# Optimization experiments

Measured on AMD Instinct MI355X. Metric: run time of the kernel, lower is better.

Reference implementation:

```python
import jax, jax.numpy as jnp
import numpy as np

VOCAB_SIZE = 256
CODEC_VOCAB = 1024  # 2 ** codec_bits
D = 1024
NHEAD = 16
FF = 4096
L = 6
ENROLLED = 225  # enrolled_codec_sec(3) * codec_rate(75)
B, TT, TA = 4, 128, 512


def sinusoidal_pe(T, d):
    pos = np.arange(T, dtype=np.float32)[:, None]
    div = np.exp(np.arange(0, d, 2, dtype=np.float32) * (-np.log(10000.0) / d))
    pe = np.zeros((T, d), dtype=np.float32)
    pe[:, 0::2] = np.sin(pos * div)
    pe[:, 1::2] = np.cos(pos * div)
    return jnp.asarray(pe)


def layernorm(x, w, b, eps=1e-5):
    mu = x.mean(-1, keepdims=True)
    var = ((x - mu) ** 2).mean(-1, keepdims=True)
    return (x - mu) * jax.lax.rsqrt(var + eps) * w + b


def mha(q_in, kv_in, in_w, in_b, out_w, out_b, mask=None):
    # q_in: [B,Tq,D], kv_in: [B,Tk,D]; mask True == blocked (torch attn_mask convention)
    d = q_in.shape[-1]
    h, hd = NHEAD, d // NHEAD
    wq, wk, wv = in_w[:d], in_w[d:2 * d], in_w[2 * d:]
    bq, bk, bv = in_b[:d], in_b[d:2 * d], in_b[2 * d:]
    Bq, Tq, _ = q_in.shape
    Tk = kv_in.shape[1]
    q = (q_in @ wq.T + bq).reshape(Bq, Tq, h, hd)
    k = (kv_in @ wk.T + bk).reshape(Bq, Tk, h, hd)
    v = (kv_in @ wv.T + bv).reshape(Bq, Tk, h, hd)
    scores = jnp.einsum('bqhd,bkhd->bhqk', q, k) / jnp.sqrt(jnp.float32(hd))
    if mask is not None:
        scores = jnp.where(mask, -jnp.inf, scores)
    attn = jax.nn.softmax(scores, axis=-1)
    o = jnp.einsum('bhqk,bkhd->bqhd', attn, v).reshape(Bq, Tq, d)
    return o @ out_w.T + out_b


def pack(te, ae, ee, tl, al):
    # Ragged concat [text[:tl]; audio[:al]; enrolled] padded to static max_len.
    Tt, Ta, Te = te.shape[0], ae.shape[0], ee.shape[0]
    pos = jnp.arange(Tt + Ta + Te)
    t = te[jnp.clip(pos, 0, Tt - 1)]
    a = ae[jnp.clip(pos - tl, 0, Ta - 1)]
    e = ee[jnp.clip(pos - tl - al, 0, Te - 1)]
    x = jnp.where((pos < tl)[:, None], t,
        jnp.where((pos < tl + al)[:, None], a,
        jnp.where((pos < tl + al + Te)[:, None], e, jnp.zeros_like(t))))
    return x


def setup_inputs():
    key = jax.random.key(0)
    ks = iter(jax.random.split(key, 64))

    def n(shape, s=0.02):
        return jax.random.normal(next(ks), shape, dtype=jnp.float32) * s

    text = jax.random.randint(next(ks), (B, TT), 0, VOCAB_SIZE)
    audio = jax.random.randint(next(ks), (B, TA), 0, CODEC_VOCAB)
    enrolled_audio = jax.random.randint(next(ks), (B, ENROLLED), 0, CODEC_VOCAB)
    # force sample 0 to full length so max_len is static (= TT+TA+ENROLLED)
    text_len_batch = jax.random.randint(next(ks), (B,), TT // 2, TT + 1).at[0].set(TT)
    audio_len_batch = jax.random.randint(next(ks), (B,), TA // 2, TA + 1).at[0].set(TA)
    return dict(
        text=text, audio=audio, enrolled_audio=enrolled_audio,
        text_len_batch=text_len_batch, audio_len_batch=audio_len_batch,
        text_emb=n((VOCAB_SIZE, D)), audio_emb=n((CODEC_VOCAB, D)),
        sa_in_w=n((L, 3 * D, D)), sa_in_b=jnp.zeros((L, 3 * D), jnp.float32),
        sa_out_w=n((L, D, D)), sa_out_b=jnp.zeros((L, D), jnp.float32),
        ca_in_w=n((L, 3 * D, D)), ca_in_b=jnp.zeros((L, 3 * D), jnp.float32),
        ca_out_w=n((L, D, D)), ca_out_b=jnp.zeros((L, D), jnp.float32),
        ff1_w=n((L, FF, D)), ff1_b=jnp.zeros((L, FF), jnp.float32),
        ff2_w=n((L, D, FF)), ff2_b=jnp.zeros((L, D), jnp.float32),
        ln1_w=jnp.ones((L, D), jnp.float32), ln1_b=jnp.zeros((L, D), jnp.float32),
        ln2_w=jnp.ones((L, D), jnp.float32), ln2_b=jnp.zeros((L, D), jnp.float32),
        ln3_w=jnp.ones((L, D), jnp.float32), ln3_b=jnp.zeros((L, D), jnp.float32),
        out_w=n((CODEC_VOCAB, D)), out_b=jnp.zeros((CODEC_VOCAB,), jnp.float32))


def reference(text, audio, enrolled_audio, text_len_batch, audio_len_batch,
              text_emb, audio_emb, sa_in_w, sa_in_b, sa_out_w, sa_out_b,
              ca_in_w, ca_in_b, ca_out_w, ca_out_b, ff1_w, ff1_b, ff2_w, ff2_b,
              ln1_w, ln1_b, ln2_w, ln2_b, ln3_w, ln3_b, out_w, out_b):
    # per-segment sinusoidal PE (positions reset at the start of each segment)
    te = text_emb[text] + sinusoidal_pe(text.shape[1], D)
    ae = audio_emb[audio] + sinusoidal_pe(audio.shape[1], D)
    ee = audio_emb[enrolled_audio] + sinusoidal_pe(enrolled_audio.shape[1], D)
    embed = jax.vmap(pack)(te, ae, ee, text_len_batch, audio_len_batch)  # [B, max_len, D]
    max_len = embed.shape[1]
    prefix = text.shape[1] + audio.shape[1]  # == max(tl+al) by construction
    mask = jnp.triu(jnp.ones((max_len, max_len), bool), 1).at[:, :prefix].set(False)
    mem = embed  # TransformerDecoder memory == embed
    x = embed
    for l in range(L):  # post-norm decoder layers (torch default norm_first=False)
        x = layernorm(x + mha(x, x, sa_in_w[l], sa_in_b[l], sa_out_w[l], sa_out_b[l], mask), ln1_w[l], ln1_b[l])
        x = layernorm(x + mha(x, mem, ca_in_w[l], ca_in_b[l], ca_out_w[l], ca_out_b[l]), ln2_w[l], ln2_b[l])
        h = jax.nn.relu(x @ ff1_w[l].T + ff1_b[l]) @ ff2_w[l].T + ff2_b[l]
        x = layernorm(x + h, ln3_w[l], ln3_b[l])
    return x @ out_w.T + out_b  # [B, max_len, CODEC_VOCAB]
```

## Files before the change

### kernel.cpp

```cpp
#include <hip/hip_runtime.h>
#include <hip/hip_bf16.h>

#define B_      4
#define TT_     128
#define TA_     512
#define TE_     225
#define T_      865
#define D_      1024
#define H_      16
#define FF_     4096
#define L_      6
#define PREFIX_ 640
#define M_TOK   (B_ * T_)
#define M_PAD   3584
#define NKV     (L_ * 2 * D_)

typedef __attribute__((ext_vector_type(8))) short          s16x8;
typedef __attribute__((ext_vector_type(4))) float          f32x4;
typedef __attribute__((ext_vector_type(8))) unsigned short u16x8;

typedef __attribute__((address_space(1))) const void gv_t;
typedef __attribute__((address_space(3))) void       lv_t;

__device__ __forceinline__ float bf2f(unsigned short u) {
  union { unsigned int i; float f; } c; c.i = ((unsigned int)u) << 16; return c.f;
}
__device__ __forceinline__ unsigned short f2bf(float f) {
  union { __hip_bfloat16 h; unsigned short u; } c; c.h = __float2bfloat16(f); return c.u;
}
template <int N> __device__ __forceinline__ void vmwait() {
  asm volatile("s_waitcnt vmcnt(%0)" :: "n"(N) : "memory");
}

__global__ __launch_bounds__(256) void embed_kernel(
    const int* __restrict__ text, const int* __restrict__ audio,
    const int* __restrict__ enrolled, const int* __restrict__ tl_b,
    const int* __restrict__ al_b, const float* __restrict__ text_emb,
    const float* __restrict__ audio_emb,
    float* __restrict__ xf, unsigned short* __restrict__ xb,
    unsigned short* __restrict__ memb, unsigned short* __restrict__ attnb) {
  int row = blockIdx.x;
  int d0 = threadIdx.x * 4;
  size_t off = (size_t)row * D_ + d0;
  if (row >= M_TOK) {
    *(unsigned long long*)&xb[off]    = 0ull;
    *(unsigned long long*)&memb[off]  = 0ull;
    *(unsigned long long*)&attnb[off] = 0ull;
    return;
  }
  int b = row / T_, pos = row - b * T_;
  int tl = tl_b[b], al = al_b[b];
  const float* emb = nullptr;
  int p = 0;
  if (pos < tl) {
    emb = text_emb + (size_t)text[b * TT_ + pos] * D_;
    p = pos;
  } else if (pos < tl + al) {
    emb = audio_emb + (size_t)audio[b * TA_ + (pos - tl)] * D_;
    p = pos - tl;
  } else if (pos < tl + al + TE_) {
    emb = audio_emb + (size_t)enrolled[b * TE_ + (pos - tl - al)] * D_;
    p = pos - tl - al;
  }
  float4 v;
  float* pv = (float*)&v;
  if (emb) {
    const float c = -9.2103403719761836f / (float)D_;
    #pragma unroll
    for (int e = 0; e < 4; ++e) {
      int d = d0 + e;
      int i = d >> 1;
      float freq = expf(c * (float)(2 * i));
      float arg = (float)p * freq;
      float pe = (d & 1) ? cosf(arg) : sinf(arg);
      pv[e] = emb[d] + pe;
    }
  } else {
    v = make_float4(0.f, 0.f, 0.f, 0.f);
  }
  *(float4*)&xf[off] = v;
  unsigned long long pk = (unsigned long long)f2bf(pv[0])
      | ((unsigned long long)f2bf(pv[1]) << 16)
      | ((unsigned long long)f2bf(pv[2]) << 32)
      | ((unsigned long long)f2bf(pv[3]) << 48);
  *(unsigned long long*)&xb[off]   = pk;
  *(unsigned long long*)&memb[off] = pk;
}

__global__ __launch_bounds__(256) void cvt_kernel(
    const float* __restrict__ in, unsigned short* __restrict__ out, int n8) {
  int i = blockIdx.x * 256 + threadIdx.x;
  if (i >= n8) return;
  const float4* pp = (const float4*)in + (size_t)i * 2;
  float4 a = pp[0], bq = pp[1];
  u16x8 o;
  o[0] = f2bf(a.x);  o[1] = f2bf(a.y);  o[2] = f2bf(a.z);  o[3] = f2bf(a.w);
  o[4] = f2bf(bq.x); o[5] = f2bf(bq.y); o[6] = f2bf(bq.z); o[7] = f2bf(bq.w);
  *(u16x8*)(out + (size_t)i * 8) = o;
}

__global__ __launch_bounds__(256) void cvt_layer_kernel(
    const float* __restrict__ s0, const float* __restrict__ s1,
    const float* __restrict__ s2, const float* __restrict__ s3,
    const float* __restrict__ s4, const float* __restrict__ s5,
    unsigned short* __restrict__ dst) {
  size_t e = ((size_t)blockIdx.x * 256 + threadIdx.x) * 8;
  if (e >= 16777216u) return;
  const float* src; size_t off;
  if      (e <  3145728u) { src = s0; off = e; }
  else if (e <  4194304u) { src = s1; off = e -  3145728u; }
  else if (e <  7340032u) { src = s2; off = e -  4194304u; }
  else if (e <  8388608u) { src = s3; off = e -  7340032u; }
  else if (e < 12582912u) { src = s4; off = e -  8388608u; }
  else                    { src = s5; off = e - 12582912u; }
  const float4* pp = (const float4*)(src + off);
  float4 a = pp[0], bq = pp[1];
  u16x8 o;
  o[0] = f2bf(a.x);  o[1] = f2bf(a.y);  o[2] = f2bf(a.z);  o[3] = f2bf(a.w);
  o[4] = f2bf(bq.x); o[5] = f2bf(bq.y); o[6] = f2bf(bq.z); o[7] = f2bf(bq.w);
  *(u16x8*)(dst + e) = o;
}

__global__ __launch_bounds__(256) void cvt_ckv_w(
    const float* __restrict__ ca_in_w, unsigned short* __restrict__ wckv) {
  int rr = blockIdx.x;
  int l = rr / (2 * D_), w = rr % (2 * D_);
  const float* src = ca_in_w + (size_t)l * 3 * D_ * D_ + (size_t)(D_ + w) * D_;
  unsigned short* dst = wckv + (size_t)rr * D_;
  int c = threadIdx.x * 4;
  float4 v4 = *(const float4*)(src + c);
  unsigned long long pk = (unsigned long long)f2bf(v4.x)
      | ((unsigned long long)f2bf(v4.y) << 16)
      | ((unsigned long long)f2bf(v4.z) << 32)
      | ((unsigned long long)f2bf(v4.w) << 48);
  *(unsigned long long*)&dst[c] = pk;
}

__global__ __launch_bounds__(256) void cvt_ckv_b(
    const float* __restrict__ ca_in_b, float* __restrict__ cbias) {
  int rr = blockIdx.x * 256 + threadIdx.x;
  if (rr >= NKV) return;
  int l = rr / (2 * D_), w = rr % (2 * D_);
  cbias[rr] = ca_in_b[(size_t)l * 3 * D_ + D_ + w];
}

template <int BM, int BN, int BK, int ACT, int OBF>
__global__ __launch_bounds__(256) void gemm_p2(
    const unsigned short* __restrict__ A, int lda,
    const unsigned short* __restrict__ W, int ldw,
    const float* __restrict__ bias,
    float* __restrict__ Cf, unsigned short* __restrict__ Cb, int ldc,
    int Mw, int K) {
  constexpr int WROWS = BM / 2, WCOLS = BN / 2;
  constexpr int WM = WROWS / 16, WN = WCOLS / 16;
  constexpr int LPR = BK / 8;
  constexpr int RPI = 64 / LPR;
  constexpr int ACH = (BM / 4) / RPI;
  constexpr int BCH = (BN / 4) / RPI;
  constexpr int ABUF = BM * BK, BBUF = BN * BK;
  constexpr int KSUB = BK / 32;
  constexpr int LW = ACH + BCH;
  __shared__ unsigned short lds[3 * (ABUF + BBUF)];

  int tid = threadIdx.x, lane = tid & 63, wid = tid >> 6;
  int gx = gridDim.x;
  int nwg = gx * gridDim.y;
  int orig = blockIdx.y * gx + blockIdx.x;
  int q = nwg >> 3, r = nwg & 7;
  int xcd = orig & 7, loc = orig >> 3;
  int wg = (xcd < r ? xcd * (q + 1) : r * (q + 1) + (xcd - r) * q) + loc;
  int m0 = (wg / gx) * BM, n0 = (wg % gx) * BN;

  int wr = wid >> 1, wc = wid & 1;
  int lrow = lane / LPR, lgrp = lane % LPR;
  int skey = (BK == 32) ? ((lrow >> 1) & 3) : (lrow & 7);
  int lk = (lgrp ^ skey) * 8;

  const unsigned short* gAp[ACH]; unsigned aoff[ACH];
  const unsigned short* gBp[BCH]; unsigned boff[BCH];
  #pragma unroll
  for (int c = 0; c < ACH; ++c) {
    int row0 = wid * (BM / 4) + c * RPI;
    gAp[c] = A + (size_t)(m0 + row0 + lrow) * lda + lk;
    aoff[c] = row0 * BK;
  }
  #pragma unroll
  for (int c = 0; c < BCH; ++c) {
    int row0 = wid * (BN / 4) + c * RPI;
    gBp[c] = W + (size_t)(n0 + row0 + lrow) * ldw + lk;
    boff[c] = row0 * BK;
  }

  f32x4 acc[WM][WN];
  #pragma unroll
  for (int i = 0; i < WM; ++i)
    #pragma unroll
    for (int j = 0; j < WN; ++j) acc[i][j] = (f32x4)0.f;

  int frow = lane & 15, g4 = lane >> 4;

  auto STAGE = [&](int bi, int t) {
    int k0 = t * BK;
    #pragma unroll
    for (int c = 0; c < ACH; ++c)
      __builtin_amdgcn_global_load_lds((gv_t*)(gAp[c] + k0),
          (lv_t*)&lds[bi * ABUF + aoff[c]], 16, 0, 0);
    #pragma unroll
    for (int c = 0; c < BCH; ++c)
      __builtin_amdgcn_global_load_lds((gv_t*)(gBp[c] + k0),
          (lv_t*)&lds[3 * ABUF + bi * BBUF + boff[c]], 16, 0, 0);
  };

  STAGE(0, 0);
  STAGE(1, 1);
  int nt = K / BK;
  int cur = 0;
  for (int t = 0; t < nt; ++t) {
    if (t + 1 < nt) vmwait<LW>(); else vmwait<0>();
    __builtin_amdgcn_s_barrier();
    if (t + 2 < nt) {
      int stb = cur + 2; if (stb >= 3) stb -= 3;
      STAGE(stb, t + 2);
    }
    const unsigned short* Ab = &lds[cur * ABUF];
    const unsigned short* Bb = &lds[3 * ABUF + cur * BBUF];
    #pragma unroll
    for (int kk = 0; kk < KSUB; ++kk) {
      int rk = (BK == 32) ? ((g4 ^ ((frow >> 1) & 3)) * 8)
                          : (((kk * 4 + g4) ^ (frow & 7)) * 8);
      s16x8 af[WM], bfr[WN];
      #pragma unroll
      for (int i = 0; i < WM; ++i)
        af[i] = *(const s16x8*)&Ab[(wr * WROWS + i * 16 + frow) * BK + rk];
      #pragma unroll
      for (int j = 0; j < WN; ++j)
        bfr[j] = *(const s16x8*)&Bb[(wc * WCOLS + j * 16 + frow) * BK + rk];
      __builtin_amdgcn_s_setprio(1);
      #pragma unroll
      for (int i = 0; i < WM; ++i)
        #pragma unroll
        for (int j = 0; j < WN; ++j)
          acc[i][j] = __builtin_amdgcn_mfma_f32_16x16x32_bf16(af[i], bfr[j], acc[i][j], 0, 0, 0);
      __builtin_amdgcn_s_setprio(0);
    }
    cur = (cur == 2) ? 0 : cur + 1;
  }

  float bv[WN];
  #pragma unroll
  for (int j = 0; j < WN; ++j) bv[j] = bias[n0 + wc * WCOLS + j * 16 + (lane & 15)];
  int rbase = m0 + wr * WROWS + (lane >> 4) * 4;
  int cbase = n0 + wc * WCOLS + (lane & 15);
  #pragma unroll
  for (int i = 0; i < WM; ++i)
    #pragma unroll
    for (int rr = 0; rr < 4; ++rr) {
      int m = rbase + i * 16 + rr;
      if (m < Mw) {
        #pragma unroll
        for (int j = 0; j < WN; ++j) {
          float v = acc[i][j][rr] + bv[j];
          if (ACT) v = fmaxf(v, 0.f);
          if (OBF) Cb[(size_t)m * ldc + cbase + j * 16] = f2bf(v);
          else     Cf[(size_t)m * ldc + cbase + j * 16] = v;
        }
      }
    }
}

template <bool MASKED>
__global__ __launch_bounds__(256) void attn_mfma(
    const unsigned short* __restrict__ qp, int qld,
    const unsigned short* __restrict__ kp,
    const unsigned short* __restrict__ vp, int kvld,
    unsigned short* __restrict__ out) {
  __shared__ unsigned short KsL[64 * 64];
  __shared__ unsigned short VtL[64 * 72];
  __shared__ unsigned short PsL[4][16 * 64];
  int tid = threadIdx.x;
  int lane = tid & 63, wid = tid >> 6;
  int b = blockIdx.y >> 4, h = blockIdx.y & 15;
  int q0 = blockIdx.x * 64;
  int r16 = lane & 15, g4 = lane >> 4;

  int qrow = q0 + wid * 16 + r16;
  if (qrow >= T_) qrow = T_ - 1;
  const unsigned short* qbase =
      qp + (size_t)(b * T_ + qrow) * qld + h * 64 + g4 * 8;
  s16x8 qf0 = *(const s16x8*)qbase;
  s16x8 qf1 = *(const s16x8*)(qbase + 32);

  float m_[4], l_[4];
  f32x4 o_[4];
  #pragma unroll
  for (int rg = 0; rg < 4; ++rg) { m_[rg] = -INFINITY; l_[rg] = 0.f; }
  #pragma unroll
  for (int dj = 0; dj < 4; ++dj) o_[dj] = (f32x4)0.f;

  const int nt = MASKED ? max(10, (int)blockIdx.x + 1) : 14;

  for (int t = 0; t < nt; ++t) {
    int k0 = t * 64;
    __syncthreads();

    #pragma unroll
    for (int c = 0; c < 2; ++c) {
      int row = wid * 16 + c * 8 + (lane >> 3);
      int kr = k0 + row; if (kr >= T_) kr = T_ - 1;
      int grp = (lane & 7) ^ (row & 7);
      const unsigned short* src =
          kp + (size_t)(b * T_ + kr) * kvld + h * 64 + grp * 8;
      __builtin_amdgcn_global_load_lds((gv_t*)src,
          (lv_t*)&KsL[(wid * 16 + c * 8) * 64], 16, 0, 0);
    }
    {
      int vkr = k0 + lane; if (vkr >= T_) vkr = T_ - 1;
      const unsigned short* vsrc =
          vp + (size_t)(b * T_ + vkr) * kvld + h * 64 + wid * 16;
      u16x8 v0 = *(const u16x8*)vsrc;
      u16x8 v1 = *(const u16x8*)(vsrc + 8);
      #pragma unroll
      for (int jj = 0; jj < 8; ++jj) {
        VtL[(wid * 16 + jj) * 72 + lane]     = v0[jj];
        VtL[(wid * 16 + 8 + jj) * 72 + lane] = v1[jj];
      }
    }
    __syncthreads();

    f32x4 sj[4];
    #pragma unroll
    for (int j = 0; j < 4; ++j) sj[j] = (f32x4)0.f;
    __builtin_amdgcn_s_setprio(1);
    #pragma unroll
    for (int j = 0; j < 4; ++j) {
      int krow = j * 16 + r16;
      s16x8 kf0 = *(const s16x8*)&KsL[krow * 64 + ((g4 ^ (krow & 7)) * 8)];
      s16x8 kf1 = *(const s16x8*)&KsL[krow * 64 + (((4 + g4) ^ (krow & 7)) * 8)];
      sj[j] = __builtin_amdgcn_mfma_f32_16x16x32_bf16(qf0, kf0, sj[j], 0, 0, 0);
      sj[j] = __builtin_amdgcn_mfma_f32_16x16x32_bf16(qf1, kf1, sj[j], 0, 0, 0);
    }
    __builtin_amdgcn_s_setprio(0);

    float alpha_[4];
    #pragma unroll
    for (int rg = 0; rg < 4; ++rg) {
      int qa = q0 + wid * 16 + g4 * 4 + rg;
      float pm = -INFINITY;
      #pragma unroll
      for (int j = 0; j < 4; ++j) {
        int kg = k0 + j * 16 + r16;
        float sv = sj[j][rg] * 0.125f;
        bool bad = (kg >= T_) || (MASKED && kg > qa && kg >= PREFIX_);
        sv = bad ? -INFINITY : sv;
        sj[j][rg] = sv;
        pm = fmaxf(pm, sv);
      }
      pm = fmaxf(pm, __shfl_xor(pm, 1));
      pm = fmaxf(pm, __shfl_xor(pm, 2));
      pm = fmaxf(pm, __shfl_xor(pm, 4));
      pm = fmaxf(pm, __shfl_xor(pm, 8));
      float mn = fmaxf(m_[rg], pm);
      float al = __expf(m_[rg] - mn);
      m_[rg] = mn;
      alpha_[rg] = al;
      int prow = g4 * 4 + rg;
      float ps = 0.f;
      #pragma unroll
      for (int j = 0; j < 4; ++j) {
        float pv = __expf(sj[j][rg] - mn);
        ps += pv;
        PsL[wid][prow * 64 + (((j * 2 + (r16 >> 3)) ^ (prow & 7)) * 8) + (r16 & 7)]
            = f2bf(pv);
      }
      ps += __shfl_xor(ps, 1);
      ps += __shfl_xor(ps, 2);
      ps += __shfl_xor(ps, 4);
      ps += __shfl_xor(ps, 8);
      l_[rg] = l_[rg] * al + ps;
    }
    #pragma unroll
    for (int dj = 0; dj < 4; ++dj)
      #pragma unroll
      for (int rg = 0; rg < 4; ++rg) o_[dj][rg] *= alpha_[rg];

    __builtin_amdgcn_s_setprio(1);
    #pragma unroll
    for (int kk = 0; kk < 2; ++kk) {
      s16x8 pf = *(const s16x8*)
          &PsL[wid][r16 * 64 + (((kk * 4 + g4) ^ (r16 & 7)) * 8)];
      #pragma unroll
      for (int dj = 0; dj < 4; ++dj) {
        s16x8 vf = *(const s16x8*)
            &VtL[(dj * 16 + r16) * 72 + kk * 32 + g4 * 8];
        o_[dj] = __builtin_amdgcn_mfma_f32_16x16x32_bf16(pf, vf, o_[dj], 0, 0, 0);
      }
    }
    __builtin_amdgcn_s_setprio(0);
  }

  #pragma unroll
  for (int rg = 0; rg < 4; ++rg) {
    int qa = q0 + wid * 16 + g4 * 4 + rg;
    if (qa < T_) {
      float inv = 1.f / l_[rg];
      unsigned short* ob = out + (size_t)(b * T_ + qa) * D_ + h * 64;
      #pragma unroll
      for (int dj = 0; dj < 4; ++dj)
        ob[dj * 16 + r16] = f2bf(o_[dj][rg] * inv);
    }
  }
}

__global__ __launch_bounds__(256) void ln_res_kernel(
    float* __restrict__ x, const float* __restrict__ r,
    const float* __restrict__ w, const float* __restrict__ b,
    unsigned short* __restrict__ xb) {
  __shared__ float red[4];
  int row = blockIdx.x, tid = threadIdx.x;
  size_t off = (size_t)row * D_ + tid * 4;
  float4 xv = *(float4*)&x[off];
  float4 rv = *(const float4*)&r[off];
  float v0 = xv.x + rv.x, v1 = xv.y + rv.y, v2 = xv.z + rv.z, v3 = xv.w + rv.w;

  float s = v0 + v1 + v2 + v3;
  #pragma unroll
  for (int o = 1; o < 64; o <<= 1) s += __shfl_xor(s, o);
  if ((tid & 63) == 0) red[tid >> 6] = s;
  __syncthreads();
  float mu = (red[0] + red[1] + red[2] + red[3]) * (1.f / 1024.f);
  __syncthreads();

  float d0 = v0 - mu, d1 = v1 - mu, d2 = v2 - mu, d3 = v3 - mu;
  float ss = d0 * d0 + d1 * d1 + d2 * d2 + d3 * d3;
  #pragma unroll
  for (int o = 1; o < 64; o <<= 1) ss += __shfl_xor(ss, o);
  if ((tid & 63) == 0) red[tid >> 6] = ss;
  __syncthreads();
  float var = (red[0] + red[1] + red[2] + red[3]) * (1.f / 1024.f);
  float rs = rsqrtf(var + 1e-5f);

  float4 wv = *(const float4*)&w[tid * 4];
  float4 bv = *(const float4*)&b[tid * 4];
  float o0 = d0 * rs * wv.x + bv.x, o1 = d1 * rs * wv.y + bv.y;
  float o2 = d2 * rs * wv.z + bv.z, o3 = d3 * rs * wv.w + bv.w;
  *(float4*)&x[off] = make_float4(o0, o1, o2, o3);
  unsigned long long pk = (unsigned long long)f2bf(o0)
      | ((unsigned long long)f2bf(o1) << 16)
      | ((unsigned long long)f2bf(o2) << 32)
      | ((unsigned long long)f2bf(o3) << 48);
  *(unsigned long long*)&xb[off] = pk;
}

extern "C" void kernel_launch(void* const* d_in, const int* in_sizes, int n_in,
                              void* d_out, int out_size, void* d_ws, size_t ws_size,
                              hipStream_t stream) {
  const int* text       = (const int*)d_in[0];
  const int* audio      = (const int*)d_in[1];
  const int* enrolled   = (const int*)d_in[2];
  const int* tl_b       = (const int*)d_in[3];
  const int* al_b       = (const int*)d_in[4];
  const float* text_emb = (const float*)d_in[5];
  const float* audio_emb= (const float*)d_in[6];
  const float* sa_in_w  = (const float*)d_in[7];
  const float* sa_in_b  = (const float*)d_in[8];
  const float* sa_out_w = (const float*)d_in[9];
  const float* sa_out_b = (const float*)d_in[10];
  const float* ca_in_w  = (const float*)d_in[11];
  const float* ca_in_b  = (const float*)d_in[12];
  const float* ca_out_w = (const float*)d_in[13];
  const float* ca_out_b = (const float*)d_in[14];
  const float* ff1_w    = (const float*)d_in[15];
  const float* ff1_b    = (const float*)d_in[16];
  const float* ff2_w    = (const float*)d_in[17];
  const float* ff2_b    = (const float*)d_in[18];
  const float* ln1_w    = (const float*)d_in[19];
  const float* ln1_b    = (const float*)d_in[20];
  const float* ln2_w    = (const float*)d_in[21];
  const float* ln2_b    = (const float*)d_in[22];
  const float* ln3_w    = (const float*)d_in[23];
  const float* ln3_b    = (const float*)d_in[24];
  const float* out_w    = (const float*)d_in[25];
  const float* out_b    = (const float*)d_in[26];

  char* p = (char*)d_ws;
  float* xf = (float*)p;            p += (size_t)M_PAD * D_ * 4;
  float* tmp = (float*)p;           p += (size_t)M_PAD * D_ * 4;
  unsigned short* xb = (unsigned short*)p;    p += (size_t)M_PAD * D_ * 2;
  unsigned short* memb = (unsigned short*)p;  p += (size_t)M_PAD * D_ * 2;
  unsigned short* qkv = (unsigned short*)p;   p += (size_t)M_PAD * FF_ * 2;
  unsigned short* attnb = (unsigned short*)p; p += (size_t)M_PAD * D_ * 2;
  unsigned short* wbuf = (unsigned short*)p;  p += (size_t)16777216 * 2;
  unsigned short* outwb = (unsigned short*)p; p += (size_t)1048576 * 2;
  unsigned short* ckv  = (unsigned short*)p;  p += (size_t)M_PAD * NKV * 2;
  unsigned short* wckv = (unsigned short*)p;  p += (size_t)NKV * D_ * 2;
  float* cbias = (float*)p;                   p += (size_t)NKV * 4;
  bool fused = ((size_t)(p - (char*)d_ws)) <= ws_size;

  unsigned short* w_sa_qkv = wbuf;
  unsigned short* w_sa_o   = wbuf + 3145728;
  unsigned short* w_ca_qkv = wbuf + 4194304;
  unsigned short* w_ca_o   = wbuf + 7340032;
  unsigned short* w_ff1    = wbuf + 8388608;
  unsigned short* w_ff2    = wbuf + 12582912;

  embed_kernel<<<M_PAD, 256, 0, stream>>>(text, audio, enrolled, tl_b, al_b,
                                          text_emb, audio_emb, xf, xb, memb, attnb);
  cvt_kernel<<<512, 256, 0, stream>>>(out_w, outwb, 131072);

  if (fused) {
    cvt_ckv_w<<<NKV, 256, 0, stream>>>(ca_in_w, wckv);
    cvt_ckv_b<<<NKV / 256, 256, 0, stream>>>(ca_in_b, cbias);
    gemm_p2<128, 128, 32, 0, 1><<<dim3(NKV / 128, M_PAD / 128), 256, 0, stream>>>(
        memb, D_, wckv, D_, cbias, nullptr, ckv, NKV, M_PAD, D_);
  }

  for (int l = 0; l < L_; ++l) {
    const float* sa_in_w_l  = sa_in_w  + (size_t)l * 3 * D_ * D_;
    const float* sa_in_b_l  = sa_in_b  + (size_t)l * 3 * D_;
    const float* sa_out_w_l = sa_out_w + (size_t)l * D_ * D_;
    const float* sa_out_b_l = sa_out_b + (size_t)l * D_;
    const float* ca_in_w_l  = ca_in_w  + (size_t)l * 3 * D_ * D_;
    const float* ca_in_b_l  = ca_in_b  + (size_t)l * 3 * D_;
    const float* ca_out_w_l = ca_out_w + (size_t)l * D_ * D_;
    const float* ca_out_b_l = ca_out_b + (size_t)l * D_;
    const float* ff1_w_l    = ff1_w    + (size_t)l * FF_ * D_;
    const float* ff1_b_l    = ff1_b    + (size_t)l * FF_;
    const float* ff2_w_l    = ff2_w    + (size_t)l * D_ * FF_;
    const float* ff2_b_l    = ff2_b    + (size_t)l * D_;

    cvt_layer_kernel<<<8192, 256, 0, stream>>>(sa_in_w_l, sa_out_w_l, ca_in_w_l,
                                               ca_out_w_l, ff1_w_l, ff2_w_l, wbuf);

    gemm_p2<128, 128, 32, 0, 1><<<dim3(3 * D_ / 128, M_PAD / 128), 256, 0, stream>>>(
        xb, D_, w_sa_qkv, D_, sa_in_b_l, nullptr, qkv, 3 * D_, M_PAD, D_);
    attn_mfma<true><<<dim3(14, B_ * H_), 256, 0, stream>>>(
        qkv, 3 * D_, qkv + D_, qkv + 2 * D_, 3 * D_, attnb);
    gemm_p2<64, 64, 64, 0, 0><<<dim3(D_ / 64, M_PAD / 64), 256, 0, stream>>>(
        attnb, D_, w_sa_o, D_, sa_out_b_l, tmp, nullptr, D_, M_PAD, D_);
    ln_res_kernel<<<M_TOK, 256, 0, stream>>>(xf, tmp, ln1_w + l * D_, ln1_b + l * D_, xb);

    gemm_p2<64, 64, 64, 0, 1><<<dim3(D_ / 64, M_PAD / 64), 256, 0, stream>>>(
        xb, D_, w_ca_qkv, D_, ca_in_b_l, nullptr, qkv, 3 * D_, M_PAD, D_);
    if (fused) {
      attn_mfma<false><<<dim3(14, B_ * H_), 256, 0, stream>>>(
          qkv, 3 * D_, ckv + (size_t)l * 2 * D_, ckv + (size_t)l * 2 * D_ + D_,
          NKV, attnb);
    } else {
      gemm_p2<64, 64, 64, 0, 1><<<dim3(2 * D_ / 64, M_PAD / 64), 256, 0, stream>>>(
          memb, D_, w_ca_qkv + (size_t)D_ * D_, D_, ca_in_b_l + D_,
          nullptr, qkv + D_, 3 * D_, M_PAD, D_);
      attn_mfma<false><<<dim3(14, B_ * H_), 256, 0, stream>>>(
          qkv, 3 * D_, qkv + D_, qkv + 2 * D_, 3 * D_, attnb);
    }
    gemm_p2<64, 64, 64, 0, 0><<<dim3(D_ / 64, M_PAD / 64), 256, 0, stream>>>(
        attnb, D_, w_ca_o, D_, ca_out_b_l, tmp, nullptr, D_, M_PAD, D_);
    ln_res_kernel<<<M_TOK, 256, 0, stream>>>(xf, tmp, ln2_w + l * D_, ln2_b + l * D_, xb);

    gemm_p2<128, 128, 32, 1, 1><<<dim3(FF_ / 128, M_PAD / 128), 256, 0, stream>>>(
        xb, D_, w_ff1, D_, ff1_b_l, nullptr, qkv, FF_, M_PAD, D_);
    gemm_p2<64, 64, 64, 0, 0><<<dim3(D_ / 64, M_PAD / 64), 256, 0, stream>>>(
        qkv, FF_, w_ff2, FF_, ff2_b_l, tmp, nullptr, D_, M_PAD, FF_);
    ln_res_kernel<<<M_TOK, 256, 0, stream>>>(xf, tmp, ln3_w + l * D_, ln3_b + l * D_, xb);
  }

  gemm_p2<64, 64, 64, 0, 0><<<dim3(D_ / 64, M_PAD / 64), 256, 0, stream>>>(
      xb, D_, outwb, D_, out_b, (float*)d_out, nullptr, D_, M_TOK, D_);
}
```

Baseline: 2.216 ms.

## Double-buffer attention K/V tiles and stripe GEMM N-tiles per XCD

The attention kernel gets double-buffered K and V shared-memory tiles. The next tile's K is fetched asynchronously into LDS and its V into registers while the current tile is computed, and the per-tile barriers drop from two to one. Separately, a template flag on the GEMM remaps workgroups so that each XCD owns a contiguous stripe of N columns, aiming to improve weight reuse in each XCD's L2 for the large-N GEMMs and FF2. This costs more LDS per attention block, which may reduce occupancy, and the remap changes tile ordering across M.

```diff
diff --git a/kernel.cpp b/kernel.cpp
--- a/kernel.cpp
+++ b/kernel.cpp
@@ -30,6 +30,9 @@
 }
 template <int N> __device__ __forceinline__ void vmwait() {
   asm volatile("s_waitcnt vmcnt(%0)" :: "n"(N) : "memory");
+}
+__device__ __forceinline__ void lgkmwait0() {
+  asm volatile("s_waitcnt lgkmcnt(0)" ::: "memory");
 }
 
 __global__ __launch_bounds__(256) void embed_kernel(
@@ -144,7 +147,7 @@
   cbias[rr] = ca_in_b[(size_t)l * 3 * D_ + D_ + w];
 }
 
-template <int BM, int BN, int BK, int ACT, int OBF>
+template <int BM, int BN, int BK, int ACT, int OBF, int NSTRIPE>
 __global__ __launch_bounds__(256) void gemm_p2(
     const unsigned short* __restrict__ A, int lda,
     const unsigned short* __restrict__ W, int ldw,
@@ -166,10 +169,19 @@
   int gx = gridDim.x;
   int nwg = gx * gridDim.y;
   int orig = blockIdx.y * gx + blockIdx.x;
-  int q = nwg >> 3, r = nwg & 7;
-  int xcd = orig & 7, loc = orig >> 3;
-  int wg = (xcd < r ? xcd * (q + 1) : r * (q + 1) + (xcd - r) * q) + loc;
-  int m0 = (wg / gx) * BM, n0 = (wg % gx) * BN;
+  int m0, n0;
+  if (NSTRIPE && (gx & 7) == 0) {
+    int stripe = gx >> 3;
+    int xcd = orig & 7, loc = orig >> 3;
+    n0 = (xcd * stripe + loc % stripe) * BN;
+    m0 = (loc / stripe) * BM;
+  } else {
+    int q = nwg >> 3, r = nwg & 7;
+    int xcd = orig & 7, loc = orig >> 3;
+    int wg = (xcd < r ? xcd * (q + 1) : r * (q + 1) + (xcd - r) * q) + loc;
+    m0 = (wg / gx) * BM;
+    n0 = (wg % gx) * BN;
+  }
 
   int wr = wid >> 1, wc = wid & 1;
   int lrow = lane / LPR, lgrp = lane % LPR;
@@ -274,8 +286,8 @@
     const unsigned short* __restrict__ kp,
     const unsigned short* __restrict__ vp, int kvld,
     unsigned short* __restrict__ out) {
-  __shared__ unsigned short KsL[64 * 64];
-  __shared__ unsigned short VtL[64 * 72];
+  __shared__ unsigned short KsL[2][64 * 64];
+  __shared__ unsigned short VtL[2][64 * 72];
   __shared__ unsigned short PsL[4][16 * 64];
   int tid = threadIdx.x;
   int lane = tid & 63, wid = tid >> 6;
@@ -299,34 +311,46 @@
 
   const int nt = MASKED ? max(10, (int)blockIdx.x + 1) : 14;
 
-  for (int t = 0; t < nt; ++t) {
-    int k0 = t * 64;
-    __syncthreads();
-
+  u16x8 vr0, vr1;
+  auto ISSUE_K = [&](int t, int bi) {
     #pragma unroll
     for (int c = 0; c < 2; ++c) {
       int row = wid * 16 + c * 8 + (lane >> 3);
-      int kr = k0 + row; if (kr >= T_) kr = T_ - 1;
+      int kr = t * 64 + row; if (kr >= T_) kr = T_ - 1;
       int grp = (lane & 7) ^ (row & 7);
       const unsigned short* src =
           kp + (size_t)(b * T_ + kr) * kvld + h * 64 + grp * 8;
       __builtin_amdgcn_global_load_lds((gv_t*)src,
-          (lv_t*)&KsL[(wid * 16 + c * 8) * 64], 16, 0, 0);
-    }
-    {
-      int vkr = k0 + lane; if (vkr >= T_) vkr = T_ - 1;
-      const unsigned short* vsrc =
-          vp + (size_t)(b * T_ + vkr) * kvld + h * 64 + wid * 16;
-      u16x8 v0 = *(const u16x8*)vsrc;
-      u16x8 v1 = *(const u16x8*)(vsrc + 8);
-      #pragma unroll
-      for (int jj = 0; jj < 8; ++jj) {
-        VtL[(wid * 16 + jj) * 72 + lane]     = v0[jj];
-        VtL[(wid * 16 + 8 + jj) * 72 + lane] = v1[jj];
-      }
-    }
-    __syncthreads();
-
+          (lv_t*)&KsL[bi][(wid * 16 + c * 8) * 64], 16, 0, 0);
+    }
+  };
+  auto ISSUE_V = [&](int t) {
+    int vkr = t * 64 + lane; if (vkr >= T_) vkr = T_ - 1;
+    const unsigned short* vsrc =
+        vp + (size_t)(b * T_ + vkr) * kvld + h * 64 + wid * 16;
+    vr0 = *(const u16x8*)vsrc;
+    vr1 = *(const u16x8*)(vsrc + 8);
+  };
+
+  ISSUE_K(0, 0);
+  ISSUE_V(0);
+
+  for (int t = 0; t < nt; ++t) {
+    int cur = t & 1;
+    vmwait<0>();
+    #pragma unroll
+    for (int jj = 0; jj < 8; ++jj) {
+      VtL[cur][(wid * 16 + jj) * 72 + lane]     = vr0[jj];
+      VtL[cur][(wid * 16 + 8 + jj) * 72 + lane] = vr1[jj];
+    }
+    lgkmwait0();
+    __builtin_amdgcn_s_barrier();
+    if (t + 1 < nt) {
+      ISSUE_K(t + 1, cur ^ 1);
+      ISSUE_V(t + 1);
+    }
+
+    int k0 = t * 64;
     f32x4 sj[4];
     #pragma unroll
     for (int j = 0; j < 4; ++j) sj[j] = (f32x4)0.f;
@@ -334,8 +358,8 @@
     #pragma unroll
     for (int j = 0; j < 4; ++j) {
       int krow = j * 16 + r16;
-      s16x8 kf0 = *(const s16x8*)&KsL[krow * 64 + ((g4 ^ (krow & 7)) * 8)];
-      s16x8 kf1 = *(const s16x8*)&KsL[krow * 64 + (((4 + g4) ^ (krow & 7)) * 8)];
+      s16x8 kf0 = *(const s16x8*)&KsL[cur][krow * 64 + ((g4 ^ (krow & 7)) * 8)];
+      s16x8 kf1 = *(const s16x8*)&KsL[cur][krow * 64 + (((4 + g4) ^ (krow & 7)) * 8)];
       sj[j] = __builtin_amdgcn_mfma_f32_16x16x32_bf16(qf0, kf0, sj[j], 0, 0, 0);
       sj[j] = __builtin_amdgcn_mfma_f32_16x16x32_bf16(qf1, kf1, sj[j], 0, 0, 0);
     }
@@ -391,7 +415,7 @@
       #pragma unroll
       for (int dj = 0; dj < 4; ++dj) {
         s16x8 vf = *(const s16x8*)
-            &VtL[(dj * 16 + r16) * 72 + kk * 32 + g4 * 8];
+            &VtL[cur][(dj * 16 + r16) * 72 + kk * 32 + g4 * 8];
         o_[dj] = __builtin_amdgcn_mfma_f32_16x16x32_bf16(pf, vf, o_[dj], 0, 0, 0);
       }
     }
@@ -510,7 +534,7 @@
   if (fused) {
     cvt_ckv_w<<<NKV, 256, 0, stream>>>(ca_in_w, wckv);
     cvt_ckv_b<<<NKV / 256, 256, 0, stream>>>(ca_in_b, cbias);
-    gemm_p2<128, 128, 32, 0, 1><<<dim3(NKV / 128, M_PAD / 128), 256, 0, stream>>>(
+    gemm_p2<128, 128, 32, 0, 1, 1><<<dim3(NKV / 128, M_PAD / 128), 256, 0, stream>>>(
         memb, D_, wckv, D_, cbias, nullptr, ckv, NKV, M_PAD, D_);
   }
 
@@ -531,38 +555,38 @@
     cvt_layer_kernel<<<8192, 256, 0, stream>>>(sa_in_w_l, sa_out_w_l, ca_in_w_l,
                                                ca_out_w_l, ff1_w_l, ff2_w_l, wbuf);
 
-    gemm_p2<128, 128, 32, 0, 1><<<dim3(3 * D_ / 128, M_PAD / 128), 256, 0, stream>>>(
+    gemm_p2<128, 128, 32, 0, 1, 1><<<dim3(3 * D_ / 128, M_PAD / 128), 256, 0, stream>>>(
         xb, D_, w_sa_qkv, D_, sa_in_b_l, nullptr, qkv, 3 * D_, M_PAD, D_);
     attn_mfma<true><<<dim3(14, B_ * H_), 256, 0, stream>>>(
         qkv, 3 * D_, qkv + D_, qkv + 2 * D_, 3 * D_, attnb);
-    gemm_p2<64, 64, 64, 0, 0><<<dim3(D_ / 64, M_PAD / 64), 256, 0, stream>>>(
+    gemm_p2<64, 64, 64, 0, 0, 0><<<dim3(D_ / 64, M_PAD / 64), 256, 0, stream>>>(
         attnb, D_, w_sa_o, D_, sa_out_b_l, tmp, nullptr, D_, M_PAD, D_);
     ln_res_kernel<<<M_TOK, 256, 0, stream>>>(xf, tmp, ln1_w + l * D_, ln1_b + l * D_, xb);
 
-    gemm_p2<64, 64, 64, 0, 1><<<dim3(D_ / 64, M_PAD / 64), 256, 0, stream>>>(
+    gemm_p2<64, 64, 64, 0, 1, 0><<<dim3(D_ / 64, M_PAD / 64), 256, 0, stream>>>(
         xb, D_, w_ca_qkv, D_, ca_in_b_l, nullptr, qkv, 3 * D_, M_PAD, D_);
     if (fused) {
       attn_mfma<false><<<dim3(14, B_ * H_), 256, 0, stream>>>(
           qkv, 3 * D_, ckv + (size_t)l * 2 * D_, ckv + (size_t)l * 2 * D_ + D_,
           NKV, attnb);
     } else {
-      gemm_p2<64, 64, 64, 0, 1><<<dim3(2 * D_ / 64, M_PAD / 64), 256, 0, stream>>>(
+      gemm_p2<64, 64, 64, 0, 1, 0><<<dim3(2 * D_ / 64, M_PAD / 64), 256, 0, stream>>>(
           memb, D_, w_ca_qkv + (size_t)D_ * D_, D_, ca_in_b_l + D_,
           nullptr, qkv + D_, 3 * D_, M_PAD, D_);
       attn_mfma<false><<<dim3(14, B_ * H_), 256, 0, stream>>>(
           qkv, 3 * D_, qkv + D_, qkv + 2 * D_, 3 * D_, attnb);
     }
-    gemm_p2<64, 64, 64, 0, 0><<<dim3(D_ / 64, M_PAD / 64), 256, 0, stream>>>(
+    gemm_p2<64, 64, 64, 0, 0, 0><<<dim3(D_ / 64, M_PAD / 64), 256, 0, stream>>>(
         attnb, D_, w_ca_o, D_, ca_out_b_l, tmp, nullptr, D_, M_PAD, D_);
     ln_res_kernel<<<M_TOK, 256, 0, stream>>>(xf, tmp, ln2_w + l * D_, ln2_b + l * D_, xb);
 
-    gemm_p2<128, 128, 32, 1, 1><<<dim3(FF_ / 128, M_PAD / 128), 256, 0, stream>>>(
+    gemm_p2<128, 128, 32, 1, 1, 1><<<dim3(FF_ / 128, M_PAD / 128), 256, 0, stream>>>(
         xb, D_, w_ff1, D_, ff1_b_l, nullptr, qkv, FF_, M_PAD, D_);
-    gemm_p2<64, 64, 64, 0, 0><<<dim3(D_ / 64, M_PAD / 64), 256, 0, stream>>>(
+    gemm_p2<64, 64, 64, 0, 0, 1><<<dim3(D_ / 64, M_PAD / 64), 256, 0, stream>>>(
         qkv, FF_, w_ff2, FF_, ff2_b_l, tmp, nullptr, D_, M_PAD, FF_);
     ln_res_kernel<<<M_TOK, 256, 0, stream>>>(xf, tmp, ln3_w + l * D_, ln3_b + l * D_, xb);
   }
 
-  gemm_p2<64, 64, 64, 0, 0><<<dim3(D_ / 64, M_PAD / 64), 256, 0, stream>>>(
+  gemm_p2<64, 64, 64, 0, 0, 0><<<dim3(D_ / 64, M_PAD / 64), 256, 0, stream>>>(
       xb, D_, outwb, D_, out_b, (float*)d_out, nullptr, D_, M_TOK, D_);
 }
```

After: 2.325 ms. +4.9%, slower.

## Add 256x256 eight-wave GEMM for wide projections and stripe N tiles per XCD

Applied to the files above, without the earlier changes.

Adds a new 512-thread GEMM kernel with 256x256 output tiles, BK=64, a double-buffered LDS pipeline fed by direct global-to-LDS loads, and s_setprio around the MFMA bursts. It is used for the self-attention QKV, cross-attention KV and FF1 projections. It also adds an optional N-striped tile-to-XCD mapping so each XCD works on a contiguous band of weight columns, enabled for the new kernel and for FF2. The goal is more operand reuse per LDS load and better L2 locality on the large GEMMs. The cost is fewer workgroups (for example 12x14 for QKV on 256 CUs), which may leave CUs idle, and heavy register pressure from 128 accumulator floats per lane.

```diff
diff --git a/kernel.cpp b/kernel.cpp
--- a/kernel.cpp
+++ b/kernel.cpp
@@ -144,7 +144,133 @@
   cbias[rr] = ca_in_b[(size_t)l * 3 * D_ + D_ + w];
 }
 
-template <int BM, int BN, int BK, int ACT, int OBF>
+template <int ACT, int OBF, int NSTRIPE>
+__global__ __launch_bounds__(512, 2) void gemm_8w(
+    const unsigned short* __restrict__ A, int lda,
+    const unsigned short* __restrict__ W, int ldw,
+    const float* __restrict__ bias,
+    float* __restrict__ Cf, unsigned short* __restrict__ Cb, int ldc,
+    int Mw, int K) {
+  __shared__ unsigned short lds[2][2][256 * 64];
+  int tid = threadIdx.x, lane = tid & 63, wid = tid >> 6;
+
+  int gx = gridDim.x;
+  int nwg = gx * gridDim.y;
+  int orig = blockIdx.y * gx + blockIdx.x;
+  int m0, n0;
+  if (NSTRIPE && (gx & 7) == 0) {
+    int stripe = gx >> 3;
+    int xcd = orig & 7, loc = orig >> 3;
+    n0 = (xcd * stripe + loc % stripe) * 256;
+    m0 = (loc / stripe) * 256;
+  } else {
+    int q = nwg >> 3, r = nwg & 7;
+    int xcd = orig & 7, loc = orig >> 3;
+    int wg = (xcd < r ? xcd * (q + 1) : r * (q + 1) + (xcd - r) * q) + loc;
+    m0 = (wg / gx) * 256;
+    n0 = (wg % gx) * 256;
+  }
+
+  int wr = wid >> 2, wc = wid & 3;
+  int r16 = lane & 15, g4 = lane >> 4;
+
+  int srow = lane >> 3;
+  int sgrp = (lane & 7) ^ srow;
+  const unsigned short* gA[4];
+  const unsigned short* gB[4];
+  unsigned soff[4];
+  #pragma unroll
+  for (int c = 0; c < 4; ++c) {
+    int rb = wid * 32 + c * 8;
+    gA[c] = A + (size_t)(m0 + rb + srow) * lda + sgrp * 8;
+    gB[c] = W + (size_t)(n0 + rb + srow) * ldw + sgrp * 8;
+    soff[c] = rb * 64;
+  }
+
+  f32x4 acc[8][4];
+  #pragma unroll
+  for (int i = 0; i < 8; ++i)
+    #pragma unroll
+    for (int j = 0; j < 4; ++j) acc[i][j] = (f32x4)0.f;
+
+  auto STAGE = [&](int bi, int t) {
+    int k0 = t * 64;
+    #pragma unroll
+    for (int c = 0; c < 4; ++c)
+      __builtin_amdgcn_global_load_lds((gv_t*)(gA[c] + k0),
+          (lv_t*)&lds[bi][0][soff[c]], 16, 0, 0);
+    #pragma unroll
+    for (int c = 0; c < 4; ++c)
+      __builtin_amdgcn_global_load_lds((gv_t*)(gB[c] + k0),
+          (lv_t*)&lds[bi][1][soff[c]], 16, 0, 0);
+  };
+
+  STAGE(0, 0);
+  int nt = K / 64, cur = 0;
+  for (int t = 0; t < nt; ++t) {
+    vmwait<0>();
+    __builtin_amdgcn_s_barrier();
+    if (t + 1 < nt) STAGE(cur ^ 1, t + 1);
+
+    const unsigned short* Ab = &lds[cur][0][0];
+    const unsigned short* Bb = &lds[cur][1][0];
+
+    s16x8 bf_[4][2];
+    #pragma unroll
+    for (int j = 0; j < 4; ++j)
+      #pragma unroll
+      for (int kk = 0; kk < 2; ++kk) {
+        int row = wc * 64 + j * 16 + r16;
+        bf_[j][kk] = *(const s16x8*)&Bb[row * 64 + (((kk * 4 + g4) ^ (row & 7)) * 8)];
+      }
+
+    #pragma unroll
+    for (int p = 0; p < 4; ++p) {
+      s16x8 af_[2][2];
+      #pragma unroll
+      for (int ii = 0; ii < 2; ++ii)
+        #pragma unroll
+        for (int kk = 0; kk < 2; ++kk) {
+          int row = wr * 128 + (p * 2 + ii) * 16 + r16;
+          af_[ii][kk] = *(const s16x8*)&Ab[row * 64 + (((kk * 4 + g4) ^ (row & 7)) * 8)];
+        }
+      __builtin_amdgcn_s_setprio(1);
+      #pragma unroll
+      for (int kk = 0; kk < 2; ++kk)
+        #pragma unroll
+        for (int ii = 0; ii < 2; ++ii)
+          #pragma unroll
+          for (int j = 0; j < 4; ++j)
+            acc[p * 2 + ii][j] = __builtin_amdgcn_mfma_f32_16x16x32_bf16(
+                af_[ii][kk], bf_[j][kk], acc[p * 2 + ii][j], 0, 0, 0);
+      __builtin_amdgcn_s_setprio(0);
+    }
+    cur ^= 1;
+  }
+
+  float bv[4];
+  #pragma unroll
+  for (int j = 0; j < 4; ++j) bv[j] = bias[n0 + wc * 64 + j * 16 + r16];
+  int rbase = m0 + wr * 128 + g4 * 4;
+  int cbase = n0 + wc * 64 + r16;
+  #pragma unroll
+  for (int i = 0; i < 8; ++i)
+    #pragma unroll
+    for (int rr = 0; rr < 4; ++rr) {
+      int m = rbase + i * 16 + rr;
+      if (m < Mw) {
+        #pragma unroll
+        for (int j = 0; j < 4; ++j) {
+          float v = acc[i][j][rr] + bv[j];
+          if (ACT) v = fmaxf(v, 0.f);
+          if (OBF) Cb[(size_t)m * ldc + cbase + j * 16] = f2bf(v);
+          else     Cf[(size_t)m * ldc + cbase + j * 16] = v;
+        }
+      }
+    }
+}
+
+template <int BM, int BN, int BK, int ACT, int OBF, int NSTRIPE>
 __global__ __launch_bounds__(256) void gemm_p2(
     const unsigned short* __restrict__ A, int lda,
     const unsigned short* __restrict__ W, int ldw,
@@ -166,10 +292,19 @@
   int gx = gridDim.x;
   int nwg = gx * gridDim.y;
   int orig = blockIdx.y * gx + blockIdx.x;
-  int q = nwg >> 3, r = nwg & 7;
-  int xcd = orig & 7, loc = orig >> 3;
-  int wg = (xcd < r ? xcd * (q + 1) : r * (q + 1) + (xcd - r) * q) + loc;
-  int m0 = (wg / gx) * BM, n0 = (wg % gx) * BN;
+  int m0, n0;
+  if (NSTRIPE && (gx & 7) == 0) {
+    int stripe = gx >> 3;
+    int xcd = orig & 7, loc = orig >> 3;
+    n0 = (xcd * stripe + loc % stripe) * BN;
+    m0 = (loc / stripe) * BM;
+  } else {
+    int q = nwg >> 3, r = nwg & 7;
+    int xcd = orig & 7, loc = orig >> 3;
+    int wg = (xcd < r ? xcd * (q + 1) : r * (q + 1) + (xcd - r) * q) + loc;
+    m0 = (wg / gx) * BM;
+    n0 = (wg % gx) * BN;
+  }
 
   int wr = wid >> 1, wc = wid & 1;
   int lrow = lane / LPR, lgrp = lane % LPR;
@@ -510,7 +645,7 @@
   if (fused) {
     cvt_ckv_w<<<NKV, 256, 0, stream>>>(ca_in_w, wckv);
     cvt_ckv_b<<<NKV / 256, 256, 0, stream>>>(ca_in_b, cbias);
-    gemm_p2<128, 128, 32, 0, 1><<<dim3(NKV / 128, M_PAD / 128), 256, 0, stream>>>(
+    gemm_8w<0, 1, 1><<<dim3(NKV / 256, M_PAD / 256), 512, 0, stream>>>(
         memb, D_, wckv, D_, cbias, nullptr, ckv, NKV, M_PAD, D_);
   }
 
@@ -531,38 +666,38 @@
     cvt_layer_kernel<<<8192, 256, 0, stream>>>(sa_in_w_l, sa_out_w_l, ca_in_w_l,
                                                ca_out_w_l, ff1_w_l, ff2_w_l, wbuf);
 
-    gemm_p2<128, 128, 32, 0, 1><<<dim3(3 * D_ / 128, M_PAD / 128), 256, 0, stream>>>(
+    gemm_8w<0, 1, 1><<<dim3(3 * D_ / 256, M_PAD / 256), 512, 0, stream>>>(
         xb, D_, w_sa_qkv, D_, sa_in_b_l, nullptr, qkv, 3 * D_, M_PAD, D_);
     attn_mfma<true><<<dim3(14, B_ * H_), 256, 0, stream>>>(
         qkv, 3 * D_, qkv + D_, qkv + 2 * D_, 3 * D_, attnb);
-    gemm_p2<64, 64, 64, 0, 0><<<dim3(D_ / 64, M_PAD / 64), 256, 0, stream>>>(
+    gemm_p2<64, 64, 64, 0, 0, 0><<<dim3(D_ / 64, M_PAD / 64), 256, 0, stream>>>(
         attnb, D_, w_sa_o, D_, sa_out_b_l, tmp, nullptr, D_, M_PAD, D_);
     ln_res_kernel<<<M_TOK, 256, 0, stream>>>(xf, tmp, ln1_w + l * D_, ln1_b + l * D_, xb);
 
-    gemm_p2<64, 64, 64, 0, 1><<<dim3(D_ / 64, M_PAD / 64), 256, 0, stream>>>(
+    gemm_p2<64, 64, 64, 0, 1, 0><<<dim3(D_ / 64, M_PAD / 64), 256, 0, stream>>>(
         xb, D_, w_ca_qkv, D_, ca_in_b_l, nullptr, qkv, 3 * D_, M_PAD, D_);
     if (fused) {
       attn_mfma<false><<<dim3(14, B_ * H_), 256, 0, stream>>>(
           qkv, 3 * D_, ckv + (size_t)l * 2 * D_, ckv + (size_t)l * 2 * D_ + D_,
           NKV, attnb);
     } else {
-      gemm_p2<64, 64, 64, 0, 1><<<dim3(2 * D_ / 64, M_PAD / 64), 256, 0, stream>>>(
+      gemm_p2<64, 64, 64, 0, 1, 0><<<dim3(2 * D_ / 64, M_PAD / 64), 256, 0, stream>>>(
           memb, D_, w_ca_qkv + (size_t)D_ * D_, D_, ca_in_b_l + D_,
           nullptr, qkv + D_, 3 * D_, M_PAD, D_);
       attn_mfma<false><<<dim3(14, B_ * H_), 256, 0, stream>>>(
           qkv, 3 * D_, qkv + D_, qkv + 2 * D_, 3 * D_, attnb);
     }
-    gemm_p2<64, 64, 64, 0, 0><<<dim3(D_ / 64, M_PAD / 64), 256, 0, stream>>>(
+    gemm_p2<64, 64, 64, 0, 0, 0><<<dim3(D_ / 64, M_PAD / 64), 256, 0, stream>>>(
         attnb, D_, w_ca_o, D_, ca_out_b_l, tmp, nullptr, D_, M_PAD, D_);
     ln_res_kernel<<<M_TOK, 256, 0, stream>>>(xf, tmp, ln2_w + l * D_, ln2_b + l * D_, xb);
 
-    gemm_p2<128, 128, 32, 1, 1><<<dim3(FF_ / 128, M_PAD / 128), 256, 0, stream>>>(
+    gemm_8w<1, 1, 1><<<dim3(FF_ / 256, M_PAD / 256), 512, 0, stream>>>(
         xb, D_, w_ff1, D_, ff1_b_l, nullptr, qkv, FF_, M_PAD, D_);
-    gemm_p2<64, 64, 64, 0, 0><<<dim3(D_ / 64, M_PAD / 64), 256, 0, stream>>>(
+    gemm_p2<64, 64, 64, 0, 0, 1><<<dim3(D_ / 64, M_PAD / 64), 256, 0, stream>>>(
         qkv, FF_, w_ff2, FF_, ff2_b_l, tmp, nullptr, D_, M_PAD, FF_);
     ln_res_kernel<<<M_TOK, 256, 0, stream>>>(xf, tmp, ln3_w + l * D_, ln3_b + l * D_, xb);
   }
 
-  gemm_p2<64, 64, 64, 0, 0><<<dim3(D_ / 64, M_PAD / 64), 256, 0, stream>>>(
+  gemm_p2<64, 64, 64, 0, 0, 0><<<dim3(D_ / 64, M_PAD / 64), 256, 0, stream>>>(
       xb, D_, outwb, D_, out_b, (float*)d_out, nullptr, D_, M_TOK, D_);
 }
```

Result: faster. 2.112 ms (-4.7%).
